# Performance work log

Measured on AMD Instinct MI355X. Metric: run time of the kernel, lower is better.

The kernel has to match this reference:

```python
import jax, jax.numpy as jnp
import numpy as np

N_ATOMS = 200_000
N_EDGES = 10_000_000
N_MOL = 128


def setup_inputs() -> dict:
    key = jax.random.key(0)
    k1, k2, k3, k4, k5, k6, k7 = jax.random.split(key, 7)
    dEdRij = jax.random.normal(k1, (N_EDGES, 3), dtype=jnp.float32)
    Rij = jax.random.normal(k2, (N_EDGES, 3), dtype=jnp.float32)
    R = jax.random.normal(k3, (N_ATOMS, 3), dtype=jnp.float32)
    # Non-degenerate cells: ~10 Angstrom cubic boxes with small perturbation
    cell = jnp.eye(3, dtype=jnp.float32) * 10.0 + 0.1 * jax.random.normal(k4, (N_MOL, 3, 3), dtype=jnp.float32)
    idx_i = jax.random.randint(k5, (N_EDGES,), 0, N_ATOMS, dtype=jnp.int32)
    idx_j = jax.random.randint(k6, (N_EDGES,), 0, N_ATOMS, dtype=jnp.int32)
    idx_m = jnp.sort(jax.random.randint(k7, (N_ATOMS,), 0, N_MOL, dtype=jnp.int32))
    return {"dEdRij": dEdRij, "Rij": Rij, "R": R, "cell": cell,
            "idx_i": idx_i, "idx_j": idx_j, "idx_m": idx_m}


def reference(dEdRij, Rij, R, cell, idx_i, idx_j, idx_m):
    N = R.shape[0]
    M = cell.shape[0]
    # Forces: F = sum_{edges into i} dE/dRij - sum_{edges from j} dE/dRij
    forces = jnp.zeros_like(R).at[idx_i].add(dEdRij).at[idx_j].add(-dEdRij)
    # Per-edge outer product [E,3,3]: Rij[:, :, None] * dEdRij[:, None, :]
    stress_edge = dEdRij[:, None, :] * Rij[:, :, None]
    # Scatter to atoms, then reduce atoms -> molecules
    stress_i = jnp.zeros((N, 3, 3), dtype=R.dtype).at[idx_i].add(stress_edge)
    stress = jax.ops.segment_sum(stress_i, idx_m, num_segments=M)  # [M,3,3]
    # Cell volume via scalar triple product a . (b x c)
    volume = jnp.sum(cell[:, 0, :] * jnp.cross(cell[:, 1, :], cell[:, 2, :]), axis=1)  # [M]
    stress_out = (stress / volume[:, None, None]).reshape(M * 3, 3)
    return forces, stress_out
```

## Files before the change

### kernel.cpp

```cpp
#include <hip/hip_runtime.h>
#include <hip/hip_bf16.h>
#include <hip/hip_fp16.h>

#define N_MOL 128
#define STRESS_FLOATS (N_MOL * 9)
#define NB 128
#define APB 1563
#define NPAD (NB * APB)
#define EPB 1024
#define K_PT 4
#define BLK 256
#define RS_SLICES 16
#define SMAX 16

__global__ void zero_f32_kernel(float* __restrict__ p, size_t n) {
    size_t i = (size_t)blockIdx.x * blockDim.x + threadIdx.x;
    if (i < n) p[i] = 0.f;
}

__device__ __forceinline__ unsigned short h16(float v) {
    return __half_as_ushort(__float2half_rn(v));
}

__global__ void __launch_bounds__(256)
scatter_kernel(const float* __restrict__ dEdRij,
               const float* __restrict__ Rij,
               const int*   __restrict__ idx_i,
               const int*   __restrict__ idx_j,
               const int*   __restrict__ idx_m,
               uint2* __restrict__ rec,
               int*   __restrict__ cnt,
               float* __restrict__ spart,
               int e0_chunk, int n_edges_chunk, int CAP)
{
    __shared__ int           hist[NB];
    __shared__ int           excl[NB];
    __shared__ int           cur[NB];
    __shared__ int           shiftb[NB];
    __shared__ float         smem[STRESS_FLOATS];
    __shared__ uint2         stg[EPB * 2];
    __shared__ unsigned char stgb[EPB * 2];

    for (int t = threadIdx.x; t < NB; t += blockDim.x) hist[t] = 0;
    for (int t = threadIdx.x; t < STRESS_FLOATS; t += blockDim.x) smem[t] = 0.f;
    __syncthreads();

    const int be0 = e0_chunk + blockIdx.x * EPB;
    const int be1 = min(be0 + EPB, e0_chunk + n_edges_chunk);

    int ei[K_PT], ej[K_PT];
    #pragma unroll
    for (int k = 0; k < K_PT; ++k) {
        const int e = be0 + k * BLK + threadIdx.x;
        ei[k] = -1; ej[k] = -1;
        if (e < be1) {
            ei[k] = idx_i[e];
            ej[k] = idx_j[e];
            atomicAdd(&hist[ei[k] / APB], 1);
            atomicAdd(&hist[ej[k] / APB], 1);
        }
    }
    __syncthreads();

    if (threadIdx.x < 64) {
        const int l = threadIdx.x;
        const int a = hist[2 * l], b = hist[2 * l + 1];
        int s = a + b;
        #pragma unroll
        for (int off = 1; off < 64; off <<= 1) {
            const int v = __shfl_up(s, off, 64);
            if (l >= off) s += v;
        }
        const int excl_pair = s - (a + b);
        excl[2 * l]     = excl_pair;
        excl[2 * l + 1] = excl_pair + a;
    }
    __syncthreads();

    for (int t = threadIdx.x; t < NB; t += blockDim.x) {
        const int h  = hist[t];
        const int ex = excl[t];
        const int g  = h ? atomicAdd(&cnt[t], h) : 0;
        cur[t]    = ex;
        shiftb[t] = t * CAP + g - ex;
    }
    __syncthreads();

    #pragma unroll
    for (int k = 0; k < K_PT; ++k) {
        const int e = be0 + k * BLK + threadIdx.x;
        if (e >= be1) continue;
        const int i = ei[k], j = ej[k];
        const float dx = dEdRij[3*e+0], dy = dEdRij[3*e+1], dz = dEdRij[3*e+2];
        const float rx = Rij[3*e+0],    ry = Rij[3*e+1],    rz = Rij[3*e+2];

        const int m = idx_m[i];
        float* s = &smem[m * 9];
        atomicAdd(&s[0], rx * dx);
        atomicAdd(&s[1], rx * dy);
        atomicAdd(&s[2], rx * dz);
        atomicAdd(&s[3], ry * dx);
        atomicAdd(&s[4], ry * dy);
        atomicAdd(&s[5], ry * dz);
        atomicAdd(&s[6], rz * dx);
        atomicAdd(&s[7], rz * dy);
        atomicAdd(&s[8], rz * dz);

        const int bi = i / APB;
        const int li = i - bi * APB;
        uint2 q;
        q.x = ((unsigned)li << 16) | h16(dx);
        q.y = (unsigned)h16(dy) | ((unsigned)h16(dz) << 16);
        int p = atomicAdd(&cur[bi], 1);
        stg[p] = q; stgb[p] = (unsigned char)bi;

        const int bj = j / APB;
        const int lj = j - bj * APB;
        q.x = ((unsigned)lj << 16) | h16(-dx);
        q.y = (unsigned)h16(-dy) | ((unsigned)h16(-dz) << 16);
        p = atomicAdd(&cur[bj], 1);
        stg[p] = q; stgb[p] = (unsigned char)bj;
    }
    __syncthreads();

    const int total = 2 * (be1 - be0);
    for (int t = threadIdx.x; t < total; t += blockDim.x) {
        const int b = stgb[t];
        const int gidx = t + shiftb[b];
        if (gidx < (b + 1) * CAP)
            rec[gidx] = stg[t];
    }

    __syncthreads();
    float* sp = spart + (size_t)blockIdx.x * STRESS_FLOATS;
    for (int t = threadIdx.x; t < STRESS_FLOATS; t += blockDim.x)
        sp[t] += smem[t];
}

__global__ void __launch_bounds__(256)
accum_kernel(const uint2* __restrict__ rec,
             const int*   __restrict__ cnt,
             float* __restrict__ partial,
             int CAP, int S)
{
    __shared__ float facc[APB * 3];
    const int b = blockIdx.x / S;
    const int s = blockIdx.x - b * S;
    for (int t = threadIdx.x; t < APB * 3; t += blockDim.x) facc[t] = 0.f;
    __syncthreads();

    int n = cnt[b];
    if (n > CAP) n = CAP;
    const int r0 = (int)((long long)n * s / S);
    const int r1 = (int)((long long)n * (s + 1) / S);
    const uint2* rb = rec + (size_t)b * CAP;

#define ACC(q)                                                        \
    {                                                                 \
        const int   l  = (int)((q).x >> 16);                          \
        const float fx = __half2float(__ushort_as_half(               \
                             (unsigned short)((q).x & 0xffffu)));     \
        const float fy = __half2float(__ushort_as_half(               \
                             (unsigned short)((q).y & 0xffffu)));     \
        const float fz = __half2float(__ushort_as_half(               \
                             (unsigned short)((q).y >> 16)));         \
        atomicAdd(&facc[l * 3 + 0], fx);                              \
        atomicAdd(&facc[l * 3 + 1], fy);                              \
        atomicAdd(&facc[l * 3 + 2], fz);                              \
    }

    int r = r0 + threadIdx.x;
    for (; r + 3 * BLK < r1; r += 4 * BLK) {
        const uint2 q0 = rb[r];
        const uint2 q1 = rb[r + BLK];
        const uint2 q2 = rb[r + 2 * BLK];
        const uint2 q3 = rb[r + 3 * BLK];
        ACC(q0); ACC(q1); ACC(q2); ACC(q3);
    }
    for (; r < r1; r += BLK) {
        const uint2 q = rb[r];
        ACC(q);
    }
#undef ACC

    __syncthreads();
    float* pp = partial + ((size_t)s * NPAD + (size_t)b * APB) * 3;
    for (int t = threadIdx.x; t < APB * 3; t += blockDim.x)
        pp[t] += facc[t];
}

__global__ void final_forces_kernel(const float* __restrict__ partial,
                                    float* __restrict__ forces, int n3, int S)
{
    const int t = blockIdx.x * blockDim.x + threadIdx.x;
    if (t >= n3) return;
    float a = 0.f;
    for (int s = 0; s < S; ++s)
        a += partial[(size_t)s * NPAD * 3 + t];
    forces[t] = a;
}

__global__ void reduce_stress_stage1(const float* __restrict__ spart,
                                     float* __restrict__ stmp, int rows)
{
    const int t = blockIdx.x * blockDim.x + threadIdx.x;
    if (t >= STRESS_FLOATS * RS_SLICES) return;
    const int col = t % STRESS_FLOATS;
    const int sl  = t / STRESS_FLOATS;
    float acc = 0.f;
    for (int r = sl; r < rows; r += RS_SLICES)
        acc += spart[(size_t)r * STRESS_FLOATS + col];
    stmp[sl * STRESS_FLOATS + col] = acc;
}

__global__ void reduce_stress_stage2(const float* __restrict__ stmp,
                                     const float* __restrict__ cell,
                                     float* __restrict__ out_stress)
{
    const int t = blockIdx.x * blockDim.x + threadIdx.x;
    if (t >= STRESS_FLOATS) return;
    float acc = 0.f;
    #pragma unroll
    for (int s = 0; s < RS_SLICES; ++s)
        acc += stmp[s * STRESS_FLOATS + t];
    const int m = t / 9;
    const float* c = &cell[m * 9];
    const float a0 = c[0], a1 = c[1], a2 = c[2];
    const float b0 = c[3], b1 = c[4], b2 = c[5];
    const float c0 = c[6], c1 = c[7], c2 = c[8];
    const float x0 = b1 * c2 - b2 * c1;
    const float x1 = b2 * c0 - b0 * c2;
    const float x2 = b0 * c1 - b1 * c0;
    const float vol = a0 * x0 + a1 * x1 + a2 * x2;
    out_stress[t] = acc / vol;
}

__global__ void zero_f64_kernel(double* __restrict__ p, int n) {
    int i = blockIdx.x * blockDim.x + threadIdx.x;
    if (i < n) p[i] = 0.0;
}

__global__ void __launch_bounds__(256)
edge_kernel_f64(const float* __restrict__ dEdRij,
                const float* __restrict__ Rij,
                const int*   __restrict__ idx_i,
                const int*   __restrict__ idx_j,
                const int*   __restrict__ idx_m,
                double* __restrict__ facc,
                float*  __restrict__ spart,
                int E)
{
    __shared__ float smem[STRESS_FLOATS];
    for (int t = threadIdx.x; t < STRESS_FLOATS; t += blockDim.x) smem[t] = 0.f;
    __syncthreads();
    const int stride = gridDim.x * blockDim.x;
    for (int e = blockIdx.x * blockDim.x + threadIdx.x; e < E; e += stride) {
        const int i = idx_i[e], j = idx_j[e];
        const float dx = dEdRij[3*e+0], dy = dEdRij[3*e+1], dz = dEdRij[3*e+2];
        const float rx = Rij[3*e+0],    ry = Rij[3*e+1],    rz = Rij[3*e+2];
        double* fi = facc + 3 * (size_t)i;
        unsafeAtomicAdd(fi + 0, (double) dx);
        unsafeAtomicAdd(fi + 1, (double) dy);
        unsafeAtomicAdd(fi + 2, (double) dz);
        double* fj = facc + 3 * (size_t)j;
        unsafeAtomicAdd(fj + 0, (double)-dx);
        unsafeAtomicAdd(fj + 1, (double)-dy);
        unsafeAtomicAdd(fj + 2, (double)-dz);
        const int m = idx_m[i];
        float* s = &smem[m * 9];
        atomicAdd(&s[0], rx*dx); atomicAdd(&s[1], rx*dy); atomicAdd(&s[2], rx*dz);
        atomicAdd(&s[3], ry*dx); atomicAdd(&s[4], ry*dy); atomicAdd(&s[5], ry*dz);
        atomicAdd(&s[6], rz*dx); atomicAdd(&s[7], rz*dy); atomicAdd(&s[8], rz*dz);
    }
    __syncthreads();
    float* sp = spart + (size_t)blockIdx.x * STRESS_FLOATS;
    for (int t = threadIdx.x; t < STRESS_FLOATS; t += blockDim.x) sp[t] = smem[t];
}

__global__ void reduce_forces_f64_kernel(const double* __restrict__ facc,
                                         float* __restrict__ forces, int n3)
{
    int t = blockIdx.x * blockDim.x + threadIdx.x;
    if (t < n3) forces[t] = (float)facc[t];
}

__global__ void reduce_stress_rows_kernel(const float* __restrict__ spart,
                                          const float* __restrict__ cell,
                                          float* __restrict__ out_stress,
                                          int rows)
{
    int t = blockIdx.x * blockDim.x + threadIdx.x;
    if (t >= STRESS_FLOATS) return;
    float acc = 0.f;
    for (int b = 0; b < rows; ++b)
        acc += spart[(size_t)b * STRESS_FLOATS + t];
    const int m = t / 9;
    const float* c = &cell[m * 9];
    const float a0 = c[0], a1 = c[1], a2 = c[2];
    const float b0 = c[3], b1 = c[4], b2 = c[5];
    const float c0 = c[6], c1 = c[7], c2 = c[8];
    const float x0 = b1*c2 - b2*c1, x1 = b2*c0 - b0*c2, x2 = b0*c1 - b1*c0;
    const float vol = a0*x0 + a1*x1 + a2*x2;
    out_stress[t] = acc / vol;
}

extern "C" void kernel_launch(void* const* d_in, const int* in_sizes, int n_in,
                              void* d_out, int out_size, void* d_ws, size_t ws_size,
                              hipStream_t stream)
{
    const float* dEdRij = (const float*)d_in[0];
    const float* Rij    = (const float*)d_in[1];
    const float* R      = (const float*)d_in[2];  (void)R;
    const float* cell   = (const float*)d_in[3];
    const int*   idx_i  = (const int*)d_in[4];
    const int*   idx_j  = (const int*)d_in[5];
    const int*   idx_m  = (const int*)d_in[6];

    const int E  = in_sizes[0] / 3;
    const int N  = in_sizes[2] / 3;
    const int n3 = N * 3;

    float* out        = (float*)d_out;
    float* forces     = out;
    float* stress_out = out + (size_t)n3;

    int nchunks = 0, SEG = 0, CAP = 0, ROWS = 0;
    size_t rec_u2 = 0, spart_f = 0;
    {
        const int cand[18][2] = {
            {2,16},{2,8},{3,16},{3,8},{2,4},{4,16},{4,8},{2,2},{3,4},
            {5,8},{6,8},{8,8},{8,4},{10,4},{16,4},{16,2},{20,2},{40,2}};
        for (int ci = 0; ci < 18; ++ci) {
            const int nc = cand[ci][0];
            const int S  = cand[ci][1];
            const int CH = (E + nc - 1) / nc;
            const long long mean = 2LL * CH / NB;
            const int cap  = (int)(mean + mean / 4 + 64);
            const int rows = (CH + EPB - 1) / EPB;
            const size_t need = (size_t)NB * cap * sizeof(uint2)
                              + (size_t)rows * STRESS_FLOATS * sizeof(float)
                              + (size_t)nc * NB * sizeof(int)
                              + (size_t)RS_SLICES * STRESS_FLOATS * sizeof(float)
                              + (size_t)S * NPAD * 3 * sizeof(float)
                              + 256;
            if (need <= ws_size) {
                nchunks = nc; SEG = S; CAP = cap; ROWS = rows;
                rec_u2  = (size_t)NB * cap;
                spart_f = (size_t)rows * STRESS_FLOATS;
                break;
            }
        }
    }

    if (nchunks > 0) {
        uint2* rec   = (uint2*)d_ws;
        float* spart = (float*)(rec + rec_u2);
        int*   cnt   = (int*)(spart + spart_f);
        float* stmp  = (float*)(cnt + (size_t)nchunks * NB);
        float* part  = stmp + (size_t)RS_SLICES * STRESS_FLOATS;

        const size_t zf = spart_f + (size_t)nchunks * NB
                        + (size_t)RS_SLICES * STRESS_FLOATS
                        + (size_t)SEG * NPAD * 3;
        zero_f32_kernel<<<(int)((zf + BLK - 1) / BLK), BLK, 0, stream>>>(
            spart, zf);

        const int CH = (E + nchunks - 1) / nchunks;
        int chunk = 0;
        for (int s = 0; s < E; s += CH, ++chunk) {
            const int ce = min(CH, E - s);
            const int nb = (ce + EPB - 1) / EPB;

            scatter_kernel<<<nb, BLK, 0, stream>>>(
                dEdRij, Rij, idx_i, idx_j, idx_m,
                rec, cnt + (size_t)chunk * NB, spart, s, ce, CAP);

            accum_kernel<<<NB * SEG, BLK, 0, stream>>>(
                rec, cnt + (size_t)chunk * NB, part, CAP, SEG);
        }

        final_forces_kernel<<<(n3 + BLK - 1) / BLK, BLK, 0, stream>>>(
            part, forces, n3, SEG);
        reduce_stress_stage1<<<(STRESS_FLOATS * RS_SLICES + BLK - 1) / BLK,
                               BLK, 0, stream>>>(spart, stmp, ROWS);
        reduce_stress_stage2<<<(STRESS_FLOATS + BLK - 1) / BLK, BLK, 0, stream>>>(
            stmp, cell, stress_out);
    } else {
        double* facc   = (double*)d_ws;
        float*  spartf = (float*)(facc + n3);

        zero_f64_kernel<<<(n3 + BLK - 1) / BLK, BLK, 0, stream>>>(facc, n3);
        edge_kernel_f64<<<2048, BLK, 0, stream>>>(
            dEdRij, Rij, idx_i, idx_j, idx_m, facc, spartf, E);
        reduce_forces_f64_kernel<<<(n3 + BLK - 1) / BLK, BLK, 0, stream>>>(
            facc, forces, n3);
        reduce_stress_rows_kernel<<<(STRESS_FLOATS + BLK - 1) / BLK, BLK, 0, stream>>>(
            spartf, cell, stress_out, 2048);
    }
}
```

Before: 1.025 ms.

## Split stress into its own grid-stride kernel and vectorize force accumulation loads

Moves the per-edge stress outer-product accumulation out of the scatter kernel into a separate persistent-grid kernel with 2048 blocks, so spart shrinks from one row per scatter block to a fixed 2048 rows. This cuts the stress reduction cost and the big zeroing kernel, since only the counters are zeroed now and the first chunk stores instead of accumulating. The accum kernel now loads records as uint4 pairs with 8-way unrolling, and CAP headroom drops from 1.25x to 1.125x the mean. The trade-off is that Rij, idx_i and idx_m are read in a separate pass, and the tighter cap raises the risk of bucket overflow.

```diff
diff --git a/kernel.cpp b/kernel.cpp
--- a/kernel.cpp
+++ b/kernel.cpp
@@ -11,11 +11,11 @@
 #define K_PT 4
 #define BLK 256
 #define RS_SLICES 16
-#define SMAX 16
-
-__global__ void zero_f32_kernel(float* __restrict__ p, size_t n) {
-    size_t i = (size_t)blockIdx.x * blockDim.x + threadIdx.x;
-    if (i < n) p[i] = 0.f;
+#define STRESS_BLOCKS 2048
+
+__global__ void zero_i32_kernel(int* __restrict__ p, int n) {
+    int i = blockIdx.x * blockDim.x + threadIdx.x;
+    if (i < n) p[i] = 0;
 }
 
 __device__ __forceinline__ unsigned short h16(float v) {
@@ -23,26 +23,57 @@
 }
 
 __global__ void __launch_bounds__(256)
+stress_kernel(const float* __restrict__ dEdRij,
+              const float* __restrict__ Rij,
+              const int*   __restrict__ idx_i,
+              const int*   __restrict__ idx_m,
+              float* __restrict__ spart,
+              int E)
+{
+    __shared__ float smem[STRESS_FLOATS];
+    for (int t = threadIdx.x; t < STRESS_FLOATS; t += blockDim.x) smem[t] = 0.f;
+    __syncthreads();
+
+    const int stride = gridDim.x * blockDim.x;
+    for (int e = blockIdx.x * blockDim.x + threadIdx.x; e < E; e += stride) {
+        const int i = idx_i[e];
+        const int m = idx_m[i];
+        const float dx = dEdRij[3*e+0], dy = dEdRij[3*e+1], dz = dEdRij[3*e+2];
+        const float rx = Rij[3*e+0],    ry = Rij[3*e+1],    rz = Rij[3*e+2];
+        float* s = &smem[m * 9];
+        atomicAdd(&s[0], rx * dx);
+        atomicAdd(&s[1], rx * dy);
+        atomicAdd(&s[2], rx * dz);
+        atomicAdd(&s[3], ry * dx);
+        atomicAdd(&s[4], ry * dy);
+        atomicAdd(&s[5], ry * dz);
+        atomicAdd(&s[6], rz * dx);
+        atomicAdd(&s[7], rz * dy);
+        atomicAdd(&s[8], rz * dz);
+    }
+
+    __syncthreads();
+    float* sp = spart + (size_t)blockIdx.x * STRESS_FLOATS;
+    for (int t = threadIdx.x; t < STRESS_FLOATS; t += blockDim.x)
+        sp[t] = smem[t];
+}
+
+__global__ void __launch_bounds__(256)
 scatter_kernel(const float* __restrict__ dEdRij,
-               const float* __restrict__ Rij,
                const int*   __restrict__ idx_i,
                const int*   __restrict__ idx_j,
-               const int*   __restrict__ idx_m,
                uint2* __restrict__ rec,
                int*   __restrict__ cnt,
-               float* __restrict__ spart,
                int e0_chunk, int n_edges_chunk, int CAP)
 {
     __shared__ int           hist[NB];
     __shared__ int           excl[NB];
     __shared__ int           cur[NB];
     __shared__ int           shiftb[NB];
-    __shared__ float         smem[STRESS_FLOATS];
     __shared__ uint2         stg[EPB * 2];
     __shared__ unsigned char stgb[EPB * 2];
 
     for (int t = threadIdx.x; t < NB; t += blockDim.x) hist[t] = 0;
-    for (int t = threadIdx.x; t < STRESS_FLOATS; t += blockDim.x) smem[t] = 0.f;
     __syncthreads();
 
     const int be0 = e0_chunk + blockIdx.x * EPB;
@@ -92,19 +123,6 @@
         if (e >= be1) continue;
         const int i = ei[k], j = ej[k];
         const float dx = dEdRij[3*e+0], dy = dEdRij[3*e+1], dz = dEdRij[3*e+2];
-        const float rx = Rij[3*e+0],    ry = Rij[3*e+1],    rz = Rij[3*e+2];
-
-        const int m = idx_m[i];
-        float* s = &smem[m * 9];
-        atomicAdd(&s[0], rx * dx);
-        atomicAdd(&s[1], rx * dy);
-        atomicAdd(&s[2], rx * dz);
-        atomicAdd(&s[3], ry * dx);
-        atomicAdd(&s[4], ry * dy);
-        atomicAdd(&s[5], ry * dz);
-        atomicAdd(&s[6], rz * dx);
-        atomicAdd(&s[7], rz * dy);
-        atomicAdd(&s[8], rz * dz);
 
         const int bi = i / APB;
         const int li = i - bi * APB;
@@ -130,18 +148,13 @@
         if (gidx < (b + 1) * CAP)
             rec[gidx] = stg[t];
     }
-
-    __syncthreads();
-    float* sp = spart + (size_t)blockIdx.x * STRESS_FLOATS;
-    for (int t = threadIdx.x; t < STRESS_FLOATS; t += blockDim.x)
-        sp[t] += smem[t];
 }
 
 __global__ void __launch_bounds__(256)
 accum_kernel(const uint2* __restrict__ rec,
              const int*   __restrict__ cnt,
              float* __restrict__ partial,
-             int CAP, int S)
+             int CAP, int S, int store)
 {
     __shared__ float facc[APB * 3];
     const int b = blockIdx.x / S;
@@ -151,42 +164,69 @@
 
     int n = cnt[b];
     if (n > CAP) n = CAP;
-    const int r0 = (int)((long long)n * s / S);
-    const int r1 = (int)((long long)n * (s + 1) / S);
+    int r0 = (int)((long long)n * s / S);
+    int r1 = (int)((long long)n * (s + 1) / S);
     const uint2* rb = rec + (size_t)b * CAP;
 
-#define ACC(q)                                                        \
+#define ACC1(w0, w1)                                                  \
     {                                                                 \
-        const int   l  = (int)((q).x >> 16);                          \
+        const int   l  = (int)((w0) >> 16);                           \
         const float fx = __half2float(__ushort_as_half(               \
-                             (unsigned short)((q).x & 0xffffu)));     \
+                             (unsigned short)((w0) & 0xffffu)));      \
         const float fy = __half2float(__ushort_as_half(               \
-                             (unsigned short)((q).y & 0xffffu)));     \
+                             (unsigned short)((w1) & 0xffffu)));      \
         const float fz = __half2float(__ushort_as_half(               \
-                             (unsigned short)((q).y >> 16)));         \
+                             (unsigned short)((w1) >> 16)));          \
         atomicAdd(&facc[l * 3 + 0], fx);                              \
         atomicAdd(&facc[l * 3 + 1], fy);                              \
         atomicAdd(&facc[l * 3 + 2], fz);                              \
     }
 
-    int r = r0 + threadIdx.x;
-    for (; r + 3 * BLK < r1; r += 4 * BLK) {
-        const uint2 q0 = rb[r];
-        const uint2 q1 = rb[r + BLK];
-        const uint2 q2 = rb[r + 2 * BLK];
-        const uint2 q3 = rb[r + 3 * BLK];
-        ACC(q0); ACC(q1); ACC(q2); ACC(q3);
-    }
-    for (; r < r1; r += BLK) {
-        const uint2 q = rb[r];
-        ACC(q);
-    }
-#undef ACC
+    if (r0 < r1 && (r0 & 1)) {
+        if (threadIdx.x == 0) { const uint2 q = rb[r0]; ACC1(q.x, q.y); }
+        ++r0;
+    }
+    if (r0 < r1 && (r1 & 1)) {
+        --r1;
+        if (threadIdx.x == 0) { const uint2 q = rb[r1]; ACC1(q.x, q.y); }
+    }
+    const int npair = (r1 - r0) >> 1;
+    const uint4* rp = (const uint4*)(rb + r0);
+
+    int p = threadIdx.x;
+    for (; p + 7 * BLK < npair; p += 8 * BLK) {
+        uint4 q0 = rp[p];
+        uint4 q1 = rp[p + 1 * BLK];
+        uint4 q2 = rp[p + 2 * BLK];
+        uint4 q3 = rp[p + 3 * BLK];
+        uint4 q4 = rp[p + 4 * BLK];
+        uint4 q5 = rp[p + 5 * BLK];
+        uint4 q6 = rp[p + 6 * BLK];
+        uint4 q7 = rp[p + 7 * BLK];
+        ACC1(q0.x, q0.y); ACC1(q0.z, q0.w);
+        ACC1(q1.x, q1.y); ACC1(q1.z, q1.w);
+        ACC1(q2.x, q2.y); ACC1(q2.z, q2.w);
+        ACC1(q3.x, q3.y); ACC1(q3.z, q3.w);
+        ACC1(q4.x, q4.y); ACC1(q4.z, q4.w);
+        ACC1(q5.x, q5.y); ACC1(q5.z, q5.w);
+        ACC1(q6.x, q6.y); ACC1(q6.z, q6.w);
+        ACC1(q7.x, q7.y); ACC1(q7.z, q7.w);
+    }
+    for (; p < npair; p += BLK) {
+        const uint4 q = rp[p];
+        ACC1(q.x, q.y); ACC1(q.z, q.w);
+    }
+#undef ACC1
 
     __syncthreads();
     float* pp = partial + ((size_t)s * NPAD + (size_t)b * APB) * 3;
-    for (int t = threadIdx.x; t < APB * 3; t += blockDim.x)
-        pp[t] += facc[t];
+    if (store) {
+        for (int t = threadIdx.x; t < APB * 3; t += blockDim.x)
+            pp[t] = facc[t];
+    } else {
+        for (int t = threadIdx.x; t < APB * 3; t += blockDim.x)
+            pp[t] += facc[t];
+    }
 }
 
 __global__ void final_forces_kernel(const float* __restrict__ partial,
@@ -284,26 +324,6 @@
     if (t < n3) forces[t] = (float)facc[t];
 }
 
-__global__ void reduce_stress_rows_kernel(const float* __restrict__ spart,
-                                          const float* __restrict__ cell,
-                                          float* __restrict__ out_stress,
-                                          int rows)
-{
-    int t = blockIdx.x * blockDim.x + threadIdx.x;
-    if (t >= STRESS_FLOATS) return;
-    float acc = 0.f;
-    for (int b = 0; b < rows; ++b)
-        acc += spart[(size_t)b * STRESS_FLOATS + t];
-    const int m = t / 9;
-    const float* c = &cell[m * 9];
-    const float a0 = c[0], a1 = c[1], a2 = c[2];
-    const float b0 = c[3], b1 = c[4], b2 = c[5];
-    const float c0 = c[6], c1 = c[7], c2 = c[8];
-    const float x0 = b1*c2 - b2*c1, x1 = b2*c0 - b0*c2, x2 = b0*c1 - b1*c0;
-    const float vol = a0*x0 + a1*x1 + a2*x2;
-    out_stress[t] = acc / vol;
-}
-
 extern "C" void kernel_launch(void* const* d_in, const int* in_sizes, int n_in,
                               void* d_out, int out_size, void* d_ws, size_t ws_size,
                               hipStream_t stream)
@@ -324,29 +344,29 @@
     float* forces     = out;
     float* stress_out = out + (size_t)n3;
 
-    int nchunks = 0, SEG = 0, CAP = 0, ROWS = 0;
-    size_t rec_u2 = 0, spart_f = 0;
+    int nchunks = 0, SEG = 0, CAP = 0;
+    size_t rec_u2 = 0;
+    const size_t spart_f = (size_t)STRESS_BLOCKS * STRESS_FLOATS;
     {
-        const int cand[18][2] = {
-            {2,16},{2,8},{3,16},{3,8},{2,4},{4,16},{4,8},{2,2},{3,4},
-            {5,8},{6,8},{8,8},{8,4},{10,4},{16,4},{16,2},{20,2},{40,2}};
-        for (int ci = 0; ci < 18; ++ci) {
+        const int cand[14][2] = {
+            {2,16},{2,8},{3,16},{3,8},{2,4},{4,8},{4,4},{2,2},
+            {5,4},{8,4},{10,2},{16,2},{20,2},{40,1}};
+        for (int ci = 0; ci < 14; ++ci) {
             const int nc = cand[ci][0];
             const int S  = cand[ci][1];
             const int CH = (E + nc - 1) / nc;
             const long long mean = 2LL * CH / NB;
-            const int cap  = (int)(mean + mean / 4 + 64);
-            const int rows = (CH + EPB - 1) / EPB;
+            int cap = (int)(mean + mean / 8 + 64);
+            cap = (cap + 1) & ~1;
             const size_t need = (size_t)NB * cap * sizeof(uint2)
-                              + (size_t)rows * STRESS_FLOATS * sizeof(float)
+                              + spart_f * sizeof(float)
                               + (size_t)nc * NB * sizeof(int)
                               + (size_t)RS_SLICES * STRESS_FLOATS * sizeof(float)
                               + (size_t)S * NPAD * 3 * sizeof(float)
                               + 256;
             if (need <= ws_size) {
-                nchunks = nc; SEG = S; CAP = cap; ROWS = rows;
+                nchunks = nc; SEG = S; CAP = cap;
                 rec_u2  = (size_t)NB * cap;
-                spart_f = (size_t)rows * STRESS_FLOATS;
                 break;
             }
         }
@@ -359,11 +379,11 @@
         float* stmp  = (float*)(cnt + (size_t)nchunks * NB);
         float* part  = stmp + (size_t)RS_SLICES * STRESS_FLOATS;
 
-        const size_t zf = spart_f + (size_t)nchunks * NB
-                        + (size_t)RS_SLICES * STRESS_FLOATS
-                        + (size_t)SEG * NPAD * 3;
-        zero_f32_kernel<<<(int)((zf + BLK - 1) / BLK), BLK, 0, stream>>>(
-            spart, zf);
+        zero_i32_kernel<<<(nchunks * NB + BLK - 1) / BLK, BLK, 0, stream>>>(
+            cnt, nchunks * NB);
+
+        stress_kernel<<<STRESS_BLOCKS, BLK, 0, stream>>>(
+            dEdRij, Rij, idx_i, idx_m, spart, E);
 
         const int CH = (E + nchunks - 1) / nchunks;
         int chunk = 0;
@@ -372,17 +392,18 @@
             const int nb = (ce + EPB - 1) / EPB;
 
             scatter_kernel<<<nb, BLK, 0, stream>>>(
-                dEdRij, Rij, idx_i, idx_j, idx_m,
-                rec, cnt + (size_t)chunk * NB, spart, s, ce, CAP);
+                dEdRij, idx_i, idx_j,
+                rec, cnt + (size_t)chunk * NB, s, ce, CAP);
 
             accum_kernel<<<NB * SEG, BLK, 0, stream>>>(
-                rec, cnt + (size_t)chunk * NB, part, CAP, SEG);
+                rec, cnt + (size_t)chunk * NB, part, CAP, SEG,
+                chunk == 0 ? 1 : 0);
         }
 
         final_forces_kernel<<<(n3 + BLK - 1) / BLK, BLK, 0, stream>>>(
             part, forces, n3, SEG);
         reduce_stress_stage1<<<(STRESS_FLOATS * RS_SLICES + BLK - 1) / BLK,
-                               BLK, 0, stream>>>(spart, stmp, ROWS);
+                               BLK, 0, stream>>>(spart, stmp, STRESS_BLOCKS);
         reduce_stress_stage2<<<(STRESS_FLOATS + BLK - 1) / BLK, BLK, 0, stream>>>(
             stmp, cell, stress_out);
     } else {
@@ -394,7 +415,9 @@
             dEdRij, Rij, idx_i, idx_j, idx_m, facc, spartf, E);
         reduce_forces_f64_kernel<<<(n3 + BLK - 1) / BLK, BLK, 0, stream>>>(
             facc, forces, n3);
-        reduce_stress_rows_kernel<<<(STRESS_FLOATS + BLK - 1) / BLK, BLK, 0, stream>>>(
-            spartf, cell, stress_out, 2048);
-    }
-}
+        reduce_stress_stage1<<<(STRESS_FLOATS * RS_SLICES + BLK - 1) / BLK,
+                               BLK, 0, stream>>>(spartf, (float*)(spartf + (size_t)2048 * STRESS_FLOATS), 2048);
+        reduce_stress_stage2<<<(STRESS_FLOATS + BLK - 1) / BLK, BLK, 0, stream>>>(
+            (float*)(spartf + (size_t)2048 * STRESS_FLOATS), cell, stress_out);
+    }
+}
```

Result: slower. 1.066 ms (+3.9%).
